# Optimization experiments

Measured on AMD Instinct MI355X. Metric: run time of the kernel, lower is better.

## Reference

```python
import jax, jax.numpy as jnp
import numpy as np

K_NEIGHBORS = 8

def _mlp(x, W0, b0, W1, b1, W2, b2, W3, b3):
    # FCBlock(hidden=128, num_hidden_layers=2, in=D+3, out=D, outermost_linear=True, with_ln=False)
    h = jax.nn.relu(x @ W0 + b0)
    h = jax.nn.relu(h @ W1 + b1)
    h = jax.nn.relu(h @ W2 + b2)
    return h @ W3 + b3


def setup_inputs() -> dict:
    key = jax.random.key(0)
    ks = jax.random.split(key, 8)
    N, M, D, H = 6890, 32768, 64, 128  # vertices, query pts, latent dim, hidden
    Din = D + 3
    sc = 0.05
    return {
        "vertex": jax.random.normal(ks[0], (N, 3), jnp.float32),
        "vertex_features": jax.random.normal(ks[1], (N, D), jnp.float32),
        "query_pts": jax.random.normal(ks[2], (M, 3), jnp.float32),
        "W0": jax.random.normal(ks[3], (Din, H), jnp.float32) * sc,
        "b0": jnp.zeros((H,), jnp.float32),
        "W1": jax.random.normal(ks[4], (H, H), jnp.float32) * sc,
        "b1": jnp.zeros((H,), jnp.float32),
        "W2": jax.random.normal(ks[5], (H, H), jnp.float32) * sc,
        "b2": jnp.zeros((H,), jnp.float32),
        "W3": jax.random.normal(ks[6], (H, D), jnp.float32) * sc,
        "b3": jnp.zeros((D,), jnp.float32),
    }


def reference(vertex, vertex_features, query_pts, W0, b0, W1, b1, W2, b2, W3, b3):
    # --- KNN: k smallest euclidean distances from each query to vertices ---
    # squared distance matrix [M, N] via the expanded form (single GEMM)
    d2 = (jnp.sum(query_pts * query_pts, axis=-1, keepdims=True)
          - 2.0 * (query_pts @ vertex.T)
          + jnp.sum(vertex * vertex, axis=-1))
    neg_d2, k_index = jax.lax.top_k(-d2, K_NEIGHBORS)  # ascending distances, [M,K]
    k_dist = jnp.sqrt(jnp.maximum(-neg_d2, 0.0)) + 1e-9
    # F.normalize(1/d, p=1, dim=1): inverse-distance weights, L1-normalized over k
    inv = 1.0 / k_dist
    k_weight = inv / jnp.sum(inv, axis=1, keepdims=True)  # [M,K]
    # --- gather neighbors ---
    k_vertices = vertex[k_index]                 # [M,K,3]
    k_nearest_features = vertex_features[k_index]  # [M,K,D]
    k_nearest_vector = query_pts[:, None, :] - k_vertices  # [M,K,3]
    vector_input = jnp.concatenate([k_nearest_features, k_nearest_vector], axis=-1)  # [M,K,D+3]
    # --- small MLP + distance-weighted reduction over neighbors ---
    features = _mlp(vector_input, W0, b0, W1, b1, W2, b2, W3, b3)  # [M,K,D]
    return jnp.sum(features * k_weight[..., None], axis=1)  # [M,D]
```

## Files before the change

kernel.cpp:

```cpp
#include <hip/hip_runtime.h>
#include <hip/hip_fp16.h>

#define NV    6890
#define NQ    32768
#define DF    64
#define NW    16
#define CHUNK 431
#define SAMP  32
#define CAPQ  20

typedef _Float16 v8h  __attribute__((ext_vector_type(8)));
typedef float    f32x4 __attribute__((ext_vector_type(4)));
typedef unsigned int       u32;
typedef unsigned long long u64;
typedef unsigned short     u16;

static constexpr size_t VTX4_OFF  = 0;
static constexpr size_t KIDX_OFF  = 110592;
static constexpr size_t KW_OFF    = KIDX_OFF + (size_t)NQ * 8 * 4;
static constexpr size_t WFRAG_OFF = KW_OFF + (size_t)NQ * 8 * 4;

__device__ __forceinline__ u32 monof(float s) {
    u32 u = __float_as_uint(s);
    return (u & 0x80000000u) ? ~u : (u | 0x80000000u);
}

__device__ __forceinline__ int sgpr(int j) {
    return __builtin_amdgcn_readfirstlane(j);
}

#define DINSERT(sv) do {                                               \
    bool c0 = (sv) < dbest[0], c1 = (sv) < dbest[1],                   \
         c2 = (sv) < dbest[2], c3 = (sv) < dbest[3],                   \
         c4 = (sv) < dbest[4], c5 = (sv) < dbest[5],                   \
         c6 = (sv) < dbest[6], c7 = (sv) < dbest[7];                   \
    dbest[7] = c7 ? (c6 ? dbest[6] : (sv)) : dbest[7];                 \
    dbest[6] = c6 ? (c5 ? dbest[5] : (sv)) : dbest[6];                 \
    dbest[5] = c5 ? (c4 ? dbest[4] : (sv)) : dbest[5];                 \
    dbest[4] = c4 ? (c3 ? dbest[3] : (sv)) : dbest[4];                 \
    dbest[3] = c3 ? (c2 ? dbest[2] : (sv)) : dbest[3];                 \
    dbest[2] = c2 ? (c1 ? dbest[1] : (sv)) : dbest[2];                 \
    dbest[1] = c1 ? (c0 ? dbest[0] : (sv)) : dbest[1];                 \
    dbest[0] = c0 ? (sv) : dbest[0];                                   \
} while (0)

#define KINSERT(nk) do {                                  \
    bool c0 = (nk) < key[0], c1 = (nk) < key[1],          \
         c2 = (nk) < key[2], c3 = (nk) < key[3],          \
         c4 = (nk) < key[4], c5 = (nk) < key[5],          \
         c6 = (nk) < key[6], c7 = (nk) < key[7];          \
    key[7] = c7 ? (c6 ? key[6] : (nk)) : key[7];          \
    key[6] = c6 ? (c5 ? key[5] : (nk)) : key[6];          \
    key[5] = c5 ? (c4 ? key[4] : (nk)) : key[5];          \
    key[4] = c4 ? (c3 ? key[3] : (nk)) : key[4];          \
    key[3] = c3 ? (c2 ? key[2] : (nk)) : key[3];          \
    key[2] = c2 ? (c1 ? key[1] : (nk)) : key[2];          \
    key[1] = c1 ? (c0 ? key[0] : (nk)) : key[1];          \
    key[0] = c0 ? (nk) : key[0];                          \
} while (0)

#define TRYQ(sv, jv) do {                                                      \
    if ((sv) <= T) {                                                           \
        if (cnt < CAPQ) { qq[w][l][cnt] = (u16)(jv); ++cnt; }                  \
        else {                                                                 \
            u64 nk = ((u64)monof(sv) << 16) | (u64)(jv);                       \
            if (nk < key[7]) { KINSERT(nk); }                                  \
        }                                                                      \
    }                                                                          \
} while (0)

__global__ void prep_kernel(const float* __restrict__ vtx, float4* __restrict__ vtx4) {
    int i = blockIdx.x * 256 + threadIdx.x;
    if (i < NV) {
        float x = vtx[i * 3 + 0], y = vtx[i * 3 + 1], z = vtx[i * 3 + 2];
        vtx4[i] = make_float4(x, y, z, 0.5f * (x * x + y * y + z * z));
    }
}

__device__ __forceinline__ float vdist(const float4 v, float nqx, float nqy, float nqz) {
    float s = fmaf(nqx, v.x, v.w);
    s = fmaf(nqy, v.y, s);
    return fmaf(nqz, v.z, s);
}

__global__ __launch_bounds__(1024, 8) void knn_kernel(const float4* __restrict__ vtx4,
                                                      const float* __restrict__ qpts,
                                                      int* __restrict__ kidx,
                                                      float* __restrict__ kw,
                                                      const float* __restrict__ W0,
                                                      const float* __restrict__ W1,
                                                      const float* __restrict__ W2,
                                                      const float* __restrict__ W3,
                                                      _Float16* __restrict__ wfrag) {
    if (blockIdx.x >= NQ / 64) {
        int e = (blockIdx.x - NQ / 64) * 1024 + threadIdx.x;
        const float* W; int base, NCT, C, KD;
        if      (e < 12288) { W = W0; base = 0;     NCT = 8; C = 128; KD = 67;  }
        else if (e < 28672) { W = W1; base = 12288; NCT = 8; C = 128; KD = 128; }
        else if (e < 45056) { W = W2; base = 28672; NCT = 8; C = 128; KD = 128; }
        else                { W = W3; base = 45056; NCT = 4; C = 64;  KD = 128; }
        int le = e - base;
        int t = le >> 9, r = le & 511;
        int lane = r >> 3, jj = r & 7;
        int kt = t / NCT, ct = t % NCT;
        int k = kt * 32 + (lane >> 4) * 8 + jj;
        int col = ct * 16 + (lane & 15);
        float v = (k < KD) ? W[k * C + col] : 0.0f;
        wfrag[e] = (_Float16)v;
        return;
    }

    __shared__ u64   kbuf[8][64][9];
    __shared__ u16   qq[NW][64][CAPQ];
    __shared__ float Tbc[64];
    float (*fbuf)[64][9] = (float (*)[64][9])kbuf;

    const int tid = threadIdx.x, w = tid >> 6, l = tid & 63;
    const int m = blockIdx.x * 64 + l;
    const float qx = qpts[m * 3 + 0], qy = qpts[m * 3 + 1], qz = qpts[m * 3 + 2];
    const float nqx = -qx, nqy = -qy, nqz = -qz;

    float dbest[8];
#pragma unroll
    for (int i = 0; i < 8; ++i) dbest[i] = 3.0e38f;
    {
        const int s0 = sgpr(w * SAMP);
#pragma unroll 4
        for (int j = 0; j < SAMP; ++j) {
            float s = vdist(vtx4[s0 + j], nqx, nqy, nqz);
            DINSERT(s);
        }
    }
#pragma unroll
    for (int i = 0; i < 8; ++i) fbuf[w][l][i] = dbest[i];
    __syncthreads();

#pragma unroll 1
    for (int st = 8; st >= 1; st >>= 1) {
        if (w < st) {
#pragma unroll
            for (int e = 0; e < 8; ++e) {
                float s = fbuf[w + st][l][e];
                if (s < dbest[7]) { DINSERT(s); }
            }
            if (st > 1) {
#pragma unroll
                for (int i = 0; i < 8; ++i) fbuf[w][l][i] = dbest[i];
            }
        }
        __syncthreads();
    }
    if (w == 0) Tbc[l] = dbest[7];
    __syncthreads();
    const float T = Tbc[l];

    u64 key[8];
#pragma unroll
    for (int i = 0; i < 8; ++i) key[i] = ~0ull;
    u32 cnt = 0;
    const int j0 = sgpr(w * CHUNK);
    const int j1 = sgpr((w * CHUNK + CHUNK < NV) ? w * CHUNK + CHUNK : NV);
    {
        int j = j0;
#pragma unroll 1
        for (; j + 4 <= j1; j += 4) {
            const int jb = sgpr(j);
            float4 v0 = vtx4[jb + 0], v1 = vtx4[jb + 1];
            float4 v2 = vtx4[jb + 2], v3 = vtx4[jb + 3];
            float s0 = vdist(v0, nqx, nqy, nqz);
            float s1 = vdist(v1, nqx, nqy, nqz);
            float s2 = vdist(v2, nqx, nqy, nqz);
            float s3 = vdist(v3, nqx, nqy, nqz);
            TRYQ(s0, jb + 0); TRYQ(s1, jb + 1); TRYQ(s2, jb + 2); TRYQ(s3, jb + 3);
        }
        for (; j < j1; ++j) {
            const int jb = sgpr(j);
            float s = vdist(vtx4[jb], nqx, nqy, nqz);
            TRYQ(s, jb);
        }
    }

#pragma unroll 1
    for (int b = 0; b < CAPQ; b += 4) {
        if (!__any(cnt > (u32)b)) break;
        u32 jj[4]; float4 vv[4];
#pragma unroll
        for (int t = 0; t < 4; ++t) {
            u32 qi = ((u32)(b + t) < cnt) ? (u32)qq[w][l][b + t] : 0u;
            jj[t] = qi; vv[t] = vtx4[qi];
        }
#pragma unroll
        for (int t = 0; t < 4; ++t) {
            float s = vdist(vv[t], nqx, nqy, nqz);
            u64 nk = ((u64)monof(s) << 16) | (u64)jj[t];
            nk = ((u32)(b + t) < cnt) ? nk : ~0ull;
            if (nk < key[7]) { KINSERT(nk); }
        }
    }

#pragma unroll 1
    for (int st = 8; st >= 1; st >>= 1) {
        if (w >= st && w < 2 * st) {
#pragma unroll
            for (int i = 0; i < 8; ++i) kbuf[w - st][l][i] = key[i];
        }
        __syncthreads();
        if (w < st) {
#pragma unroll
            for (int e = 0; e < 8; ++e) {
                u64 nk = kbuf[w][l][e];
                if (nk < key[7]) { KINSERT(nk); }
            }
        }
        __syncthreads();
    }

    if (w == 0) {
        float q2 = fmaf(qx, qx, fmaf(qy, qy, qz * qz));
        float inv[8], ssum = 0.0f;
        int idx8[8];
#pragma unroll
        for (int i = 0; i < 8; ++i) {
            u32 us = (u32)(key[i] >> 16);
            u32 uo = (us & 0x80000000u) ? (us & 0x7FFFFFFFu) : ~us;
            float s = __uint_as_float(uo);
            float dd = fmaf(2.0f, s, q2);
            float d = sqrtf(fmaxf(dd, 0.0f)) + 1e-9f;
            inv[i] = 1.0f / d; ssum += inv[i];
            idx8[i] = (int)(key[i] & 0xFFFFull);
        }
        float rs = 1.0f / ssum;
#pragma unroll
        for (int i = 0; i < 8; ++i) {
            kidx[m * 8 + i] = idx8[i];
            kw[m * 8 + i]   = inv[i] * rs;
        }
    }
}

template <int KSTEPS, int NCT, bool RELU>
__device__ __forceinline__ void mlp_layer(_Float16 (*buf)[136],
                                          const _Float16* __restrict__ frag,
                                          const float* __restrict__ bias,
                                          int w, int l) {
    const int cl = l & 15, gl = l >> 4;
    f32x4 acc[2][NCT];
#pragma unroll
    for (int ct = 0; ct < NCT; ++ct) {
        float bv = bias[ct * 16 + cl];
#pragma unroll
        for (int rt = 0; rt < 2; ++rt) acc[rt][ct] = (f32x4){bv, bv, bv, bv};
    }
    const _Float16* fb = frag + (size_t)l * 8;
#pragma unroll 1
    for (int ks = 0; ks < KSTEPS; ++ks) {
        v8h a0 = *(const v8h*)&buf[w * 32 + cl][ks * 32 + gl * 8];
        v8h a1 = *(const v8h*)&buf[w * 32 + 16 + cl][ks * 32 + gl * 8];
#pragma unroll
        for (int ct = 0; ct < NCT; ++ct) {
            v8h bf = *(const v8h*)(fb + (size_t)(ks * NCT + ct) * 512);
            acc[0][ct] = __builtin_amdgcn_mfma_f32_16x16x32_f16(a0, bf, acc[0][ct], 0, 0, 0);
            acc[1][ct] = __builtin_amdgcn_mfma_f32_16x16x32_f16(a1, bf, acc[1][ct], 0, 0, 0);
        }
    }
#pragma unroll
    for (int rt = 0; rt < 2; ++rt)
#pragma unroll
        for (int ct = 0; ct < NCT; ++ct)
#pragma unroll
            for (int j = 0; j < 4; ++j) {
                float v = acc[rt][ct][j];
                if (RELU) v = fmaxf(v, 0.0f);
                buf[w * 32 + rt * 16 + gl * 4 + j][ct * 16 + cl] = (_Float16)v;
            }
}

__global__ __launch_bounds__(256, 3) void mlp_kernel(
    const float* __restrict__ vf, const float4* __restrict__ vtx4,
    const float* __restrict__ qpts,
    const int* __restrict__ kidx, const float* __restrict__ kw,
    const _Float16* __restrict__ wfrag,
    const float* __restrict__ b0, const float* __restrict__ b1,
    const float* __restrict__ b2, const float* __restrict__ b3,
    float* __restrict__ out) {
    __shared__ _Float16 buf[128][136];
    const int tid = threadIdx.x, w = tid >> 6, l = tid & 63;
    {
        int h = l & 1;
        int lrow = w * 32 + (l >> 1);
        int grow = blockIdx.x * 128 + lrow;
        int q = grow >> 3;
        int idx = kidx[grow];
        const float4* src = (const float4*)(vf + (size_t)idx * DF) + h * 8;
#pragma unroll
        for (int t = 0; t < 4; ++t) {
            float4 a = src[2 * t], b = src[2 * t + 1];
            v8h pk = {(_Float16)a.x, (_Float16)a.y, (_Float16)a.z, (_Float16)a.w,
                      (_Float16)b.x, (_Float16)b.y, (_Float16)b.z, (_Float16)b.w};
            *(v8h*)&buf[lrow][h * 32 + t * 8] = pk;
        }
        v8h zz = {0, 0, 0, 0, 0, 0, 0, 0};
        if (h == 0) {
            float4 v = vtx4[idx];
            float qx = qpts[q * 3 + 0], qy = qpts[q * 3 + 1], qz = qpts[q * 3 + 2];
            v8h d = {(_Float16)(qx - v.x), (_Float16)(qy - v.y), (_Float16)(qz - v.z),
                     0, 0, 0, 0, 0};
            *(v8h*)&buf[lrow][64] = d;
            *(v8h*)&buf[lrow][88] = zz;
        } else {
            *(v8h*)&buf[lrow][72] = zz;
            *(v8h*)&buf[lrow][80] = zz;
        }
    }

    mlp_layer<3, 8, true>(buf, wfrag + 0,     b0, w, l);
    mlp_layer<4, 8, true>(buf, wfrag + 12288, b1, w, l);
    mlp_layer<4, 8, true>(buf, wfrag + 28672, b2, w, l);

    {
        const int cl = l & 15, gl = l >> 4;
        f32x4 acc[2][4];
#pragma unroll
        for (int ct = 0; ct < 4; ++ct) {
            float bv = b3[ct * 16 + cl];
#pragma unroll
            for (int rt = 0; rt < 2; ++rt) acc[rt][ct] = (f32x4){bv, bv, bv, bv};
        }
        const _Float16* fb = wfrag + 45056 + (size_t)l * 8;
#pragma unroll 1
        for (int ks = 0; ks < 4; ++ks) {
            v8h a0 = *(const v8h*)&buf[w * 32 + cl][ks * 32 + gl * 8];
            v8h a1 = *(const v8h*)&buf[w * 32 + 16 + cl][ks * 32 + gl * 8];
#pragma unroll
            for (int ct = 0; ct < 4; ++ct) {
                v8h bf = *(const v8h*)(fb + (size_t)(ks * 4 + ct) * 512);
                acc[0][ct] = __builtin_amdgcn_mfma_f32_16x16x32_f16(a0, bf, acc[0][ct], 0, 0, 0);
                acc[1][ct] = __builtin_amdgcn_mfma_f32_16x16x32_f16(a1, bf, acc[1][ct], 0, 0, 0);
            }
        }
        int GRbase = blockIdx.x * 128 + w * 32;
#pragma unroll
        for (int rt = 0; rt < 2; ++rt) {
            int r4 = GRbase + rt * 16 + gl * 4;
            float4 kv = *(const float4*)&kw[r4];
#pragma unroll
            for (int ct = 0; ct < 4; ++ct) {
                float v = acc[rt][ct][0] * kv.x + acc[rt][ct][1] * kv.y +
                          acc[rt][ct][2] * kv.z + acc[rt][ct][3] * kv.w;
                v += __shfl_xor(v, 16);
                if ((gl & 1) == 0) {
                    int q = (GRbase + rt * 16 + ((gl == 2) ? 8 : 0)) >> 3;
                    out[(size_t)q * 64 + ct * 16 + cl] = v;
                }
            }
        }
    }
}

extern "C" void kernel_launch(void* const* d_in, const int* in_sizes, int n_in,
                              void* d_out, int out_size, void* d_ws, size_t ws_size,
                              hipStream_t stream) {
    const float* vtx = (const float*)d_in[0];
    const float* vf  = (const float*)d_in[1];
    const float* qp  = (const float*)d_in[2];
    const float* W0  = (const float*)d_in[3];
    const float* b0  = (const float*)d_in[4];
    const float* W1  = (const float*)d_in[5];
    const float* b1  = (const float*)d_in[6];
    const float* W2  = (const float*)d_in[7];
    const float* b2  = (const float*)d_in[8];
    const float* W3  = (const float*)d_in[9];
    const float* b3  = (const float*)d_in[10];
    float*       out = (float*)d_out;

    char*      ws    = (char*)d_ws;
    float4*    vtx4  = (float4*)(ws + VTX4_OFF);
    int*       kidx  = (int*)(ws + KIDX_OFF);
    float*     kw    = (float*)(ws + KW_OFF);
    _Float16*  wfrag = (_Float16*)(ws + WFRAG_OFF);

    hipLaunchKernelGGL(prep_kernel, dim3(27), dim3(256), 0, stream, vtx, vtx4);
    hipLaunchKernelGGL(knn_kernel, dim3(NQ / 64 + 52), dim3(1024), 0, stream,
                       vtx4, qp, kidx, kw, W0, W1, W2, W3, wfrag);
    hipLaunchKernelGGL(mlp_kernel, dim3(NQ * 8 / 128), dim3(256), 0, stream,
                       vf, vtx4, qp, kidx, kw, wfrag, b0, b1, b2, b3, out);
}
```

Baseline: 151.9 us.

## Stage MLP weight fragments through shared memory in column-tile halves

Reorders the packed weight fragments to be column-tile-major so each half of a layer's output columns is contiguous. The MLP kernel then copies each half into a 16 KB shared-memory buffer cooperatively and reads B fragments from LDS instead of from global/L2 per wave. This is meant to cut redundant global weight loads across the four waves, at the cost of extra block barriers, copy time and more LDS per block, which may reduce occupancy.

After: 157.0 us. 1.03x slower.

```diff
diff --git a/kernel.cpp b/kernel.cpp
--- a/kernel.cpp
+++ b/kernel.cpp
@@ -94,15 +94,15 @@
                                                       _Float16* __restrict__ wfrag) {
     if (blockIdx.x >= NQ / 64) {
         int e = (blockIdx.x - NQ / 64) * 1024 + threadIdx.x;
-        const float* W; int base, NCT, C, KD;
-        if      (e < 12288) { W = W0; base = 0;     NCT = 8; C = 128; KD = 67;  }
-        else if (e < 28672) { W = W1; base = 12288; NCT = 8; C = 128; KD = 128; }
-        else if (e < 45056) { W = W2; base = 28672; NCT = 8; C = 128; KD = 128; }
-        else                { W = W3; base = 45056; NCT = 4; C = 64;  KD = 128; }
+        const float* W; int base, C, KD, KS;
+        if      (e < 12288) { W = W0; base = 0;     C = 128; KD = 67;  KS = 3; }
+        else if (e < 28672) { W = W1; base = 12288; C = 128; KD = 128; KS = 4; }
+        else if (e < 45056) { W = W2; base = 28672; C = 128; KD = 128; KS = 4; }
+        else                { W = W3; base = 45056; C = 64;  KD = 128; KS = 4; }
         int le = e - base;
         int t = le >> 9, r = le & 511;
         int lane = r >> 3, jj = r & 7;
-        int kt = t / NCT, ct = t % NCT;
+        int ct = t / KS, kt = t % KS;
         int k = kt * 32 + (lane >> 4) * 8 + jj;
         int col = ct * 16 + (lane & 15);
         float v = (k < KD) ? W[k * C + col] : 0.0f;
@@ -238,35 +238,58 @@
     }
 }
 
-template <int KSTEPS, int NCT, bool RELU>
-__device__ __forceinline__ void mlp_layer(_Float16 (*buf)[136],
-                                          const _Float16* __restrict__ frag,
-                                          const float* __restrict__ bias,
-                                          int w, int l) {
+__device__ __forceinline__ void stage_w(_Float16* wst, const _Float16* __restrict__ src,
+                                        int nt, int tid) {
+    const v8h* s = (const v8h*)src;
+    v8h*       d = (v8h*)wst;
+    for (int p = tid; p < nt * 64; p += 256) d[p] = s[p];
+}
+
+template <int KSTEPS, bool RELU>
+__device__ __forceinline__ void mlp_layer8(_Float16 (*buf)[136], _Float16* wst,
+                                           const _Float16* __restrict__ frag,
+                                           const float* __restrict__ bias,
+                                           int w, int l, int tid) {
     const int cl = l & 15, gl = l >> 4;
-    f32x4 acc[2][NCT];
-#pragma unroll
-    for (int ct = 0; ct < NCT; ++ct) {
+    f32x4 acc[2][8];
+#pragma unroll
+    for (int ct = 0; ct < 8; ++ct) {
         float bv = bias[ct * 16 + cl];
-#pragma unroll
-        for (int rt = 0; rt < 2; ++rt) acc[rt][ct] = (f32x4){bv, bv, bv, bv};
-    }
-    const _Float16* fb = frag + (size_t)l * 8;
+        acc[0][ct] = (f32x4){bv, bv, bv, bv};
+        acc[1][ct] = (f32x4){bv, bv, bv, bv};
+    }
+    __syncthreads();
+    stage_w(wst, frag, 4 * KSTEPS, tid);
+    __syncthreads();
 #pragma unroll 1
     for (int ks = 0; ks < KSTEPS; ++ks) {
         v8h a0 = *(const v8h*)&buf[w * 32 + cl][ks * 32 + gl * 8];
         v8h a1 = *(const v8h*)&buf[w * 32 + 16 + cl][ks * 32 + gl * 8];
 #pragma unroll
-        for (int ct = 0; ct < NCT; ++ct) {
-            v8h bf = *(const v8h*)(fb + (size_t)(ks * NCT + ct) * 512);
-            acc[0][ct] = __builtin_amdgcn_mfma_f32_16x16x32_f16(a0, bf, acc[0][ct], 0, 0, 0);
-            acc[1][ct] = __builtin_amdgcn_mfma_f32_16x16x32_f16(a1, bf, acc[1][ct], 0, 0, 0);
+        for (int c = 0; c < 4; ++c) {
+            v8h bf = *(const v8h*)&wst[(c * KSTEPS + ks) * 512 + l * 8];
+            acc[0][c] = __builtin_amdgcn_mfma_f32_16x16x32_f16(a0, bf, acc[0][c], 0, 0, 0);
+            acc[1][c] = __builtin_amdgcn_mfma_f32_16x16x32_f16(a1, bf, acc[1][c], 0, 0, 0);
+        }
+    }
+    __syncthreads();
+    stage_w(wst, frag + (size_t)4 * KSTEPS * 512, 4 * KSTEPS, tid);
+    __syncthreads();
+#pragma unroll 1
+    for (int ks = 0; ks < KSTEPS; ++ks) {
+        v8h a0 = *(const v8h*)&buf[w * 32 + cl][ks * 32 + gl * 8];
+        v8h a1 = *(const v8h*)&buf[w * 32 + 16 + cl][ks * 32 + gl * 8];
+#pragma unroll
+        for (int c = 0; c < 4; ++c) {
+            v8h bf = *(const v8h*)&wst[(c * KSTEPS + ks) * 512 + l * 8];
+            acc[0][4 + c] = __builtin_amdgcn_mfma_f32_16x16x32_f16(a0, bf, acc[0][4 + c], 0, 0, 0);
+            acc[1][4 + c] = __builtin_amdgcn_mfma_f32_16x16x32_f16(a1, bf, acc[1][4 + c], 0, 0, 0);
         }
     }
 #pragma unroll
     for (int rt = 0; rt < 2; ++rt)
 #pragma unroll
-        for (int ct = 0; ct < NCT; ++ct)
+        for (int ct = 0; ct < 8; ++ct)
 #pragma unroll
             for (int j = 0; j < 4; ++j) {
                 float v = acc[rt][ct][j];
@@ -284,6 +307,7 @@
     const float* __restrict__ b2, const float* __restrict__ b3,
     float* __restrict__ out) {
     __shared__ _Float16 buf[128][136];
+    __shared__ _Float16 wst[8192];
     const int tid = threadIdx.x, w = tid >> 6, l = tid & 63;
     {
         int h = l & 1;
@@ -313,9 +337,9 @@
         }
     }
 
-    mlp_layer<3, 8, true>(buf, wfrag + 0,     b0, w, l);
-    mlp_layer<4, 8, true>(buf, wfrag + 12288, b1, w, l);
-    mlp_layer<4, 8, true>(buf, wfrag + 28672, b2, w, l);
+    mlp_layer8<3, true>(buf, wst, wfrag + 0,     b0, w, l, tid);
+    mlp_layer8<4, true>(buf, wst, wfrag + 12288, b1, w, l, tid);
+    mlp_layer8<4, true>(buf, wst, wfrag + 28672, b2, w, l, tid);
 
     {
         const int cl = l & 15, gl = l >> 4;
@@ -326,14 +350,16 @@
 #pragma unroll
             for (int rt = 0; rt < 2; ++rt) acc[rt][ct] = (f32x4){bv, bv, bv, bv};
         }
-        const _Float16* fb = wfrag + 45056 + (size_t)l * 8;
+        __syncthreads();
+        stage_w(wst, wfrag + 45056, 16, tid);
+        __syncthreads();
 #pragma unroll 1
         for (int ks = 0; ks < 4; ++ks) {
             v8h a0 = *(const v8h*)&buf[w * 32 + cl][ks * 32 + gl * 8];
             v8h a1 = *(const v8h*)&buf[w * 32 + 16 + cl][ks * 32 + gl * 8];
 #pragma unroll
             for (int ct = 0; ct < 4; ++ct) {
-                v8h bf = *(const v8h*)(fb + (size_t)(ks * 4 + ct) * 512);
+                v8h bf = *(const v8h*)&wst[(ct * 4 + ks) * 512 + l * 8];
                 acc[0][ct] = __builtin_amdgcn_mfma_f32_16x16x32_f16(a0, bf, acc[0][ct], 0, 0, 0);
                 acc[1][ct] = __builtin_amdgcn_mfma_f32_16x16x32_f16(a1, bf, acc[1][ct], 0, 0, 0);
             }
```
